# Kernel tuning notes

Measured on AMD Instinct MI355X. Metric: run time of the kernel, lower is better.

## Reference

```python
import jax, jax.numpy as jnp
import numpy as np

EPS = 1e-8  # matches F.cosine_similarity default eps


def setup_inputs() -> dict:
    key = jax.random.key(0)
    k1, k2, k3 = jax.random.split(key, 3)
    B, C, H, W = 16, 256, 64, 64
    n_e = 1024
    z = jax.random.normal(k1, (B, C, H, W), dtype=jnp.float32)
    gt = jax.random.normal(k2, (B, C, H, W), dtype=jnp.float32)
    codebook = jax.random.normal(k3, (n_e, C), dtype=jnp.float32)
    return {"z": z, "gt": gt, "codebook": codebook}


def _sq_dist(x, cb):
    return (jnp.sum(x * x, axis=1, keepdims=True)
            + jnp.sum(cb * cb, axis=1)
            - 2.0 * x @ cb.T)


def reference(z, gt, codebook):
    B, C, H, W = z.shape
    # permute to (B,H,W,C) then flatten to (N, e_dim)
    zf = jnp.transpose(z, (0, 2, 3, 1)).reshape(-1, C)
    gf = jnp.transpose(gt, (0, 2, 3, 1)).reshape(-1, C)

    idx = jnp.argmin(_sq_dist(zf, codebook), axis=1)       # [N]
    idx_gt = jnp.argmin(_sq_dist(gf, codebook), axis=1)    # [N]

    # one-hot @ codebook == direct gather
    z_q = codebook[idx].reshape(B, H, W, C)
    z_q_gt = codebook[idx_gt].reshape(B, H, W, C)

    # F.cosine_similarity(z_q_gt, z_q, dim=1) on (B,H,W,C): reduces over H -> (B,W,C)
    num = jnp.sum(z_q_gt * z_q, axis=1)
    nx = jnp.maximum(jnp.sqrt(jnp.sum(z_q_gt * z_q_gt, axis=1)), EPS)
    ny = jnp.maximum(jnp.sqrt(jnp.sum(z_q * z_q, axis=1)), EPS)
    cosine_score = num / (nx * ny)                         # (B, W, C)

    return cosine_score, idx_gt[:, None], idx[:, None]
```

## Files before the change

### kernel.cpp

```cpp
#include <hip/hip_runtime.h>

typedef _Float16 f16x8 __attribute__((ext_vector_type(8)));
typedef float f32x4 __attribute__((ext_vector_type(4)));

#define CDIM 256
#define NE 1024
#define HW 4096
#define CHW 1048576
#define OUT_COS 262144
#define N_PIX 65536
#define NT 32
#define TAU 0.1f

#define XROW_DW 260
#define XS_DW   (16 * XROW_DW)


__global__ void prep_kernel(const float* __restrict__ cb,
                            _Float16* __restrict__ hi,
                            float* __restrict__ c2f,
                            double* __restrict__ c2d) {
    int code = blockIdx.x;
    int lane = threadIdx.x;
    int t = code >> 5, sub = (code >> 4) & 1, n = code & 15;
    const float* row = cb + code * CDIM;
    double s = 0.0;
    #pragma unroll
    for (int i = 0; i < 4; ++i) {
        int d = i * 64 + lane;
        float x = row[d];
        s += (double)x * (double)x;
        int f = d >> 5, q = (d >> 3) & 3, r = d & 7;
        hi[(size_t)t * 8192 + sub * 4096 + f * 512 + q * 128 + n * 8 + r] =
            (_Float16)x;
    }
    #pragma unroll
    for (int off = 32; off > 0; off >>= 1)
        s += __shfl_down(s, off, 64);
    if (lane == 0) { c2f[code] = (float)(0.5 * s); c2d[code] = 0.5 * s; }
}

__device__ __forceinline__ void gl_lds16(const void* g, void* l) {
    __builtin_amdgcn_global_load_lds(
        (const __attribute__((address_space(1))) unsigned int*)g,
        (__attribute__((address_space(3))) unsigned int*)l, 16, 0, 0);
}

__launch_bounds__(256, 2)
__global__ void argmin_kernel(const float* __restrict__ Z,
                              const float* __restrict__ GT,
                              const _Float16* __restrict__ ghi,
                              const float* __restrict__ cb,
                              const float* __restrict__ c2f,
                              const double* __restrict__ c2d,
                              float* __restrict__ out_z,
                              float* __restrict__ out_gt) {
    __shared__ __align__(16) char smem[2 * 16640 + 4096 + 1024];
    float*    xs   = (float*)smem;
    _Float16* lbuf = (_Float16*)smem;
    float*    c2s  = (float*)(smem + 33280);
    int*      cand = (int*)(smem + 37376);

    const int wave = threadIdx.x >> 6;
    const int lane = threadIdx.x & 63;
    const int l15 = lane & 15;
    const int quad = lane >> 4;
    const int half = blockIdx.x >> 8;
    const float* X = half ? GT : Z;
    float* out_idx = half ? out_gt : out_z;
    const int p0 = (blockIdx.x & 255) * 256;

    #pragma unroll
    for (int i = 0; i < 4; ++i)
        c2s[i * 256 + threadIdx.x] = c2f[i * 256 + threadIdx.x];

    const float* xsrc = X + (size_t)(p0 >> 12) * CHW + (p0 & 4095);

    auto stage_x = [&](int b, int fr) {
        #pragma unroll
        for (int i = 0; i < 4; ++i) {
            const int rr = wave * 4 + i;
            const int d = fr * 16 + rr;
            gl_lds16(xsrc + (size_t)d * HW + lane * 4,
                     xs + b * XS_DW + rr * XROW_DW);
        }
    };

    f16x8 nah[4][8];
    stage_x(0, 0);
    int xb = 0;
    #pragma unroll
    for (int fr = 0; fr < 16; ++fr) {
        __syncthreads();
        if (fr < 15) stage_x(xb ^ 1, fr + 1);
        if ((quad >> 1) == (fr & 1)) {
            const int f = fr >> 1;
            const float* xsb = xs + xb * XS_DW;
            const int abase = (quad & 1) * 8 * XROW_DW + wave * 64 + l15;
            #pragma unroll
            for (int g = 0; g < 4; ++g) {
                f16x8 tv;
                #pragma unroll
                for (int j = 0; j < 8; ++j)
                    tv[j] = -(_Float16)xsb[abase + j * XROW_DW + g * 16];
                nah[g][f] = tv;
            }
        }
        xb ^= 1;
    }
    __syncthreads();

    int b1[4][4], b2[4][4];
    #pragma unroll
    for (int g = 0; g < 4; ++g)
        #pragma unroll
        for (int r = 0; r < 4; ++r) { b1[g][r] = 0x7fffffff; b2[g][r] = 0x7fffffff; }

    auto stage = [&](int b, int t) {
        #pragma unroll
        for (int i = 0; i < 4; ++i) {
            const int c = wave * 4 + i;
            gl_lds16(ghi + (size_t)t * 8192 + c * 512 + lane * 8,
                     lbuf + b * 8192 + c * 512);
        }
    };

    stage(0, 0);
    __syncthreads();

    for (int t = 0; t < NT; ++t) {
        const int cur = t & 1;
        if (t < NT - 1) stage(cur ^ 1, t + 1);

        #pragma unroll
        for (int sub = 0; sub < 2; ++sub) {
            const int n = t * 32 + sub * 16 + l15;
            const float c2 = c2s[n];
            f32x4 acc[4];
            #pragma unroll
            for (int g = 0; g < 4; ++g)
                acc[g] = (f32x4){c2, c2, c2, c2};

            #pragma unroll
            for (int f = 0; f < 8; ++f) {
                f16x8 bh = *(const f16x8*)&lbuf[cur * 8192 + sub * 4096 + f * 512 + lane * 8];
                acc[0] = __builtin_amdgcn_mfma_f32_16x16x32_f16(nah[0][f], bh, acc[0], 0, 0, 0);
                acc[1] = __builtin_amdgcn_mfma_f32_16x16x32_f16(nah[1][f], bh, acc[1], 0, 0, 0);
                acc[2] = __builtin_amdgcn_mfma_f32_16x16x32_f16(nah[2][f], bh, acc[2], 0, 0, 0);
                acc[3] = __builtin_amdgcn_mfma_f32_16x16x32_f16(nah[3][f], bh, acc[3], 0, 0, 0);
            }

            #pragma unroll
            for (int g = 0; g < 4; ++g) {
                #pragma unroll
                for (int r = 0; r < 4; ++r) {
                    int k = (__float_as_int(acc[g][r]) & 0xFFFFFC00) | n;
                    int mx = max(b1[g][r], k);
                    b2[g][r] = min(b2[g][r], mx);
                    b1[g][r] = min(b1[g][r], k);
                }
            }
        }
        __syncthreads();
    }

    #pragma unroll
    for (int g = 0; g < 4; ++g) {
        #pragma unroll
        for (int r = 0; r < 4; ++r) {
            int x1 = b1[g][r], x2 = b2[g][r];
            #pragma unroll
            for (int off = 8; off > 0; off >>= 1) {
                int o1 = __shfl_xor(x1, off, 64);
                int o2 = __shfl_xor(x2, off, 64);
                int tt = max(x1, o1);
                x2 = min(min(x2, o2), tt);
                x1 = min(x1, o1);
            }
            if (l15 == 0) {
                const int i1 = x1 & 1023, i2 = x2 & 1023;
                const float s1 = __int_as_float(x1 & 0xFFFFFC00);
                const float s2 = __int_as_float(x2 & 0xFFFFFC00);
                const int row = quad * 4 + r;
                const int slot = g * 16 + row;
                const bool flag = (s2 - s1) < TAU;
                cand[wave * 64 + slot] = i1 | (i2 << 10) | (flag ? (1 << 20) : 0);
                if (!flag) out_idx[p0 + wave * 64 + slot] = (float)i1;
            }
        }
    }

    const int info = cand[wave * 64 + lane];
    if (info & (1 << 20)) {
        const int i1 = info & 1023, i2 = (info >> 10) & 1023;
        const int p = p0 + wave * 64 + lane;
        const float* xb2 = X + (size_t)(p >> 12) * CHW + (p & 4095);
        const float* r1 = cb + (size_t)i1 * CDIM;
        const float* r2 = cb + (size_t)i2 * CDIM;
        double d1 = 0.0, d2 = 0.0;
        #pragma unroll 4
        for (int d = 0; d < CDIM; d += 4) {
            float x0 = xb2[(size_t)(d + 0) * HW];
            float x1v = xb2[(size_t)(d + 1) * HW];
            float x2v = xb2[(size_t)(d + 2) * HW];
            float x3v = xb2[(size_t)(d + 3) * HW];
            const float4 v1 = *(const float4*)(r1 + d);
            const float4 v2 = *(const float4*)(r2 + d);
            d1 += (double)x0 * v1.x + (double)x1v * v1.y
                + (double)x2v * v1.z + (double)x3v * v1.w;
            d2 += (double)x0 * v2.x + (double)x1v * v2.y
                + (double)x2v * v2.z + (double)x3v * v2.w;
        }
        const double dd1 = c2d[i1] - d1;
        const double dd2 = c2d[i2] - d2;
        const int bi = (dd2 < dd1 || (dd2 == dd1 && i2 < i1)) ? i2 : i1;
        out_idx[p] = (float)bi;
    }
}

__global__ void cosine_kernel(const float* __restrict__ cb,
                              const float* __restrict__ idx_z_f,
                              const float* __restrict__ idx_gt_f,
                              float* __restrict__ out_cos) {
    __shared__ int s_ig[64], s_iq[64];
    const int bw = blockIdx.x;
    const int c = threadIdx.x;
    const int b = bw >> 6, w = bw & 63;
    if (c < 64) {
        s_ig[c] = (int)idx_gt_f[b * 4096 + c * 64 + w];
    } else if (c < 128) {
        int h = c - 64;
        s_iq[h] = (int)idx_z_f[b * 4096 + h * 64 + w];
    }
    __syncthreads();
    float num = 0.f, sa = 0.f, sb = 0.f;
    #pragma unroll 1
    for (int h = 0; h < 64; h += 4) {
        float av[4], bv[4];
        #pragma unroll
        for (int u = 0; u < 4; ++u) {
            av[u] = cb[s_ig[h + u] * CDIM + c];
            bv[u] = cb[s_iq[h + u] * CDIM + c];
        }
        #pragma unroll
        for (int u = 0; u < 4; ++u) {
            num += av[u] * bv[u];
            sa += av[u] * av[u];
            sb += bv[u] * bv[u];
        }
    }
    const float nx = fmaxf(sqrtf(sa), 1e-8f);
    const float ny = fmaxf(sqrtf(sb), 1e-8f);
    out_cos[bw * CDIM + c] = num / (nx * ny);
}

extern "C" void kernel_launch(void* const* d_in, const int* in_sizes, int n_in,
                              void* d_out, int out_size, void* d_ws, size_t ws_size,
                              hipStream_t stream) {
    const float* z  = (const float*)d_in[0];
    const float* gt = (const float*)d_in[1];
    const float* cb = (const float*)d_in[2];
    float* out = (float*)d_out;

    _Float16* hi = (_Float16*)d_ws;
    float*  c2f = (float*)((char*)d_ws + 512 * 1024);
    double* c2d = (double*)((char*)d_ws + 516 * 1024);

    float* out_cos    = out;
    float* out_idx_gt = out + OUT_COS;
    float* out_idx_z  = out + OUT_COS + N_PIX;

    prep_kernel<<<NE, 64, 0, stream>>>(cb, hi, c2f, c2d);
    argmin_kernel<<<512, 256, 0, stream>>>(z, gt, hi, cb, c2f, c2d,
                                           out_idx_z, out_idx_gt);
    cosine_kernel<<<1024, 256, 0, stream>>>(cb, out_idx_z, out_idx_gt, out_cos);
}
```

Baseline: 229.0 us.

## Split codebook scan across two wave groups per block and merge top-2

```diff
diff --git a/kernel.cpp b/kernel.cpp
--- a/kernel.cpp
+++ b/kernel.cpp
@@ -9,7 +9,7 @@
 #define CHW 1048576
 #define OUT_COS 262144
 #define N_PIX 65536
-#define NT 32
+#define NTH 16
 #define TAU 0.1f
 
 #define XROW_DW 260
@@ -46,7 +46,7 @@
         (__attribute__((address_space(3))) unsigned int*)l, 16, 0, 0);
 }
 
-__launch_bounds__(256, 2)
+__launch_bounds__(512, 2)
 __global__ void argmin_kernel(const float* __restrict__ Z,
                               const float* __restrict__ GT,
                               const _Float16* __restrict__ ghi,
@@ -55,34 +55,38 @@
                               const double* __restrict__ c2d,
                               float* __restrict__ out_z,
                               float* __restrict__ out_gt) {
-    __shared__ __align__(16) char smem[2 * 16640 + 4096 + 1024];
-    float*    xs   = (float*)smem;
-    _Float16* lbuf = (_Float16*)smem;
-    float*    c2s  = (float*)(smem + 33280);
-    int*      cand = (int*)(smem + 37376);
-
-    const int wave = threadIdx.x >> 6;
-    const int lane = threadIdx.x & 63;
-    const int l15 = lane & 15;
+    __shared__ __align__(16) char smem[65536 + 4096 + 2048 + 2048];
+    float*    xs    = (float*)smem;
+    _Float16* lbuf  = (_Float16*)smem;
+    float*    c2s   = (float*)(smem + 65536);
+    int*      cand1 = (int*)(smem + 69632);
+    int*      cand2 = (int*)(smem + 71680);
+
+    const int tid  = threadIdx.x;
+    const int wave = tid >> 6;
+    const int lane = tid & 63;
+    const int l15  = lane & 15;
     const int quad = lane >> 4;
-    const int half = blockIdx.x >> 8;
-    const float* X = half ? GT : Z;
-    float* out_idx = half ? out_gt : out_z;
+    const int pw   = wave & 3;
+    const int ch   = wave >> 2;
+    const int inp  = blockIdx.x >> 8;
+    const float* X = inp ? GT : Z;
+    float* out_idx = inp ? out_gt : out_z;
     const int p0 = (blockIdx.x & 255) * 256;
 
     #pragma unroll
-    for (int i = 0; i < 4; ++i)
-        c2s[i * 256 + threadIdx.x] = c2f[i * 256 + threadIdx.x];
+    for (int i = 0; i < 2; ++i)
+        c2s[i * 512 + tid] = c2f[i * 512 + tid];
 
     const float* xsrc = X + (size_t)(p0 >> 12) * CHW + (p0 & 4095);
 
     auto stage_x = [&](int b, int fr) {
         #pragma unroll
-        for (int i = 0; i < 4; ++i) {
-            const int rr = wave * 4 + i;
+        for (int i = 0; i < 2; ++i) {
+            const int rr = wave * 2 + i;
             const int d = fr * 16 + rr;
             gl_lds16(xsrc + (size_t)d * HW + lane * 4,
-                     xs + b * XS_DW + rr * XROW_DW);
+                     xs + b * (XS_DW / 1) + rr * XROW_DW);
         }
     };
 
@@ -96,7 +100,7 @@
         if ((quad >> 1) == (fr & 1)) {
             const int f = fr >> 1;
             const float* xsb = xs + xb * XS_DW;
-            const int abase = (quad & 1) * 8 * XROW_DW + wave * 64 + l15;
+            const int abase = (quad & 1) * 8 * XROW_DW + pw * 64 + l15;
             #pragma unroll
             for (int g = 0; g < 4; ++g) {
                 f16x8 tv;
@@ -119,22 +123,22 @@
     auto stage = [&](int b, int t) {
         #pragma unroll
         for (int i = 0; i < 4; ++i) {
-            const int c = wave * 4 + i;
-            gl_lds16(ghi + (size_t)t * 8192 + c * 512 + lane * 8,
-                     lbuf + b * 8192 + c * 512);
+            const int c = pw * 4 + i;
+            gl_lds16(ghi + (size_t)(ch * NTH + t) * 8192 + c * 512 + lane * 8,
+                     lbuf + (ch * 2 + b) * 8192 + c * 512);
         }
     };
 
     stage(0, 0);
     __syncthreads();
 
-    for (int t = 0; t < NT; ++t) {
+    for (int t = 0; t < NTH; ++t) {
         const int cur = t & 1;
-        if (t < NT - 1) stage(cur ^ 1, t + 1);
+        if (t < NTH - 1) stage(cur ^ 1, t + 1);
 
         #pragma unroll
         for (int sub = 0; sub < 2; ++sub) {
-            const int n = t * 32 + sub * 16 + l15;
+            const int n = ch * 512 + t * 32 + sub * 16 + l15;
             const float c2 = c2s[n];
             f32x4 acc[4];
             #pragma unroll
@@ -143,7 +147,8 @@
 
             #pragma unroll
             for (int f = 0; f < 8; ++f) {
-                f16x8 bh = *(const f16x8*)&lbuf[cur * 8192 + sub * 4096 + f * 512 + lane * 8];
+                f16x8 bh = *(const f16x8*)
+                    &lbuf[(ch * 2 + cur) * 8192 + sub * 4096 + f * 512 + lane * 8];
                 acc[0] = __builtin_amdgcn_mfma_f32_16x16x32_f16(nah[0][f], bh, acc[0], 0, 0, 0);
                 acc[1] = __builtin_amdgcn_mfma_f32_16x16x32_f16(nah[1][f], bh, acc[1], 0, 0, 0);
                 acc[2] = __builtin_amdgcn_mfma_f32_16x16x32_f16(nah[2][f], bh, acc[2], 0, 0, 0);
@@ -178,43 +183,50 @@
                 x1 = min(x1, o1);
             }
             if (l15 == 0) {
-                const int i1 = x1 & 1023, i2 = x2 & 1023;
-                const float s1 = __int_as_float(x1 & 0xFFFFFC00);
-                const float s2 = __int_as_float(x2 & 0xFFFFFC00);
                 const int row = quad * 4 + r;
-                const int slot = g * 16 + row;
-                const bool flag = (s2 - s1) < TAU;
-                cand[wave * 64 + slot] = i1 | (i2 << 10) | (flag ? (1 << 20) : 0);
-                if (!flag) out_idx[p0 + wave * 64 + slot] = (float)i1;
-            }
-        }
-    }
-
-    const int info = cand[wave * 64 + lane];
-    if (info & (1 << 20)) {
-        const int i1 = info & 1023, i2 = (info >> 10) & 1023;
-        const int p = p0 + wave * 64 + lane;
-        const float* xb2 = X + (size_t)(p >> 12) * CHW + (p & 4095);
-        const float* r1 = cb + (size_t)i1 * CDIM;
-        const float* r2 = cb + (size_t)i2 * CDIM;
-        double d1 = 0.0, d2 = 0.0;
-        #pragma unroll 4
-        for (int d = 0; d < CDIM; d += 4) {
-            float x0 = xb2[(size_t)(d + 0) * HW];
-            float x1v = xb2[(size_t)(d + 1) * HW];
-            float x2v = xb2[(size_t)(d + 2) * HW];
-            float x3v = xb2[(size_t)(d + 3) * HW];
-            const float4 v1 = *(const float4*)(r1 + d);
-            const float4 v2 = *(const float4*)(r2 + d);
-            d1 += (double)x0 * v1.x + (double)x1v * v1.y
-                + (double)x2v * v1.z + (double)x3v * v1.w;
-            d2 += (double)x0 * v2.x + (double)x1v * v2.y
-                + (double)x2v * v2.z + (double)x3v * v2.w;
-        }
-        const double dd1 = c2d[i1] - d1;
-        const double dd2 = c2d[i2] - d2;
-        const int bi = (dd2 < dd1 || (dd2 == dd1 && i2 < i1)) ? i2 : i1;
-        out_idx[p] = (float)bi;
+                const int px = pw * 64 + g * 16 + row;
+                cand1[ch * 256 + px] = x1;
+                cand2[ch * 256 + px] = x2;
+            }
+        }
+    }
+    __syncthreads();
+
+    if (tid < 256) {
+        const int px = tid;
+        const int a1 = cand1[px],       a2 = cand2[px];
+        const int c1 = cand1[256 + px], c2k = cand2[256 + px];
+        const int m1 = min(a1, c1);
+        const int m2 = min(min(a2, c2k), max(a1, c1));
+        const int i1 = m1 & 1023, i2 = m2 & 1023;
+        const float s1 = __int_as_float(m1 & 0xFFFFFC00);
+        const float s2 = __int_as_float(m2 & 0xFFFFFC00);
+        const int p = p0 + px;
+        if ((s2 - s1) >= TAU) {
+            out_idx[p] = (float)i1;
+        } else {
+            const float* xb2 = X + (size_t)(p >> 12) * CHW + (p & 4095);
+            const float* r1 = cb + (size_t)i1 * CDIM;
+            const float* r2 = cb + (size_t)i2 * CDIM;
+            double d1 = 0.0, d2 = 0.0;
+            #pragma unroll 4
+            for (int d = 0; d < CDIM; d += 4) {
+                float x0 = xb2[(size_t)(d + 0) * HW];
+                float x1v = xb2[(size_t)(d + 1) * HW];
+                float x2v = xb2[(size_t)(d + 2) * HW];
+                float x3v = xb2[(size_t)(d + 3) * HW];
+                const float4 v1 = *(const float4*)(r1 + d);
+                const float4 v2 = *(const float4*)(r2 + d);
+                d1 += (double)x0 * v1.x + (double)x1v * v1.y
+                    + (double)x2v * v1.z + (double)x3v * v1.w;
+                d2 += (double)x0 * v2.x + (double)x1v * v2.y
+                    + (double)x2v * v2.z + (double)x3v * v2.w;
+            }
+            const double dd1 = c2d[i1] - d1;
+            const double dd2 = c2d[i2] - d2;
+            const int bi = (dd2 < dd1 || (dd2 == dd1 && i2 < i1)) ? i2 : i1;
+            out_idx[p] = (float)bi;
+        }
     }
 }
 
@@ -271,7 +283,7 @@
     float* out_idx_z  = out + OUT_COS + N_PIX;
 
     prep_kernel<<<NE, 64, 0, stream>>>(cb, hi, c2f, c2d);
-    argmin_kernel<<<512, 256, 0, stream>>>(z, gt, hi, cb, c2f, c2d,
+    argmin_kernel<<<512, 512, 0, stream>>>(z, gt, hi, cb, c2f, c2d,
                                            out_idx_z, out_idx_gt);
     cosine_kernel<<<1024, 256, 0, stream>>>(cb, out_idx_z, out_idx_gt, out_cos);
 }
```

Result: slower. 239.7 us (+4.7%).

## Triple-buffer LDS staging with vmcnt waits and a single barrier per step

Applied to the files above, without the earlier changes.

```diff
diff --git a/kernel.cpp b/kernel.cpp
--- a/kernel.cpp
+++ b/kernel.cpp
@@ -13,7 +13,7 @@
 #define TAU 0.1f
 
 #define XROW_DW 260
-#define XS_DW   (16 * XROW_DW)
+#define XS_DW   4160
 
 
 __global__ void prep_kernel(const float* __restrict__ cb,
@@ -55,11 +55,11 @@
                               const double* __restrict__ c2d,
                               float* __restrict__ out_z,
                               float* __restrict__ out_gt) {
-    __shared__ __align__(16) char smem[2 * 16640 + 4096 + 1024];
+    __shared__ __align__(16) char smem[55040];
     float*    xs   = (float*)smem;
     _Float16* lbuf = (_Float16*)smem;
-    float*    c2s  = (float*)(smem + 33280);
-    int*      cand = (int*)(smem + 37376);
+    float*    c2s  = (float*)(smem + 49920);
+    int*      cand = (int*)(smem + 54016);
 
     const int wave = threadIdx.x >> 6;
     const int lane = threadIdx.x & 63;
@@ -88,14 +88,19 @@
 
     f16x8 nah[4][8];
     stage_x(0, 0);
-    int xb = 0;
     #pragma unroll
     for (int fr = 0; fr < 16; ++fr) {
-        __syncthreads();
-        if (fr < 15) stage_x(xb ^ 1, fr + 1);
+        if (fr < 15) {
+            stage_x((fr + 1) % 3, fr + 1);
+            asm volatile("s_waitcnt vmcnt(4)" ::: "memory");
+        } else {
+            asm volatile("s_waitcnt vmcnt(0)" ::: "memory");
+        }
+        __builtin_amdgcn_s_barrier();
+        __builtin_amdgcn_sched_barrier(0);
         if ((quad >> 1) == (fr & 1)) {
             const int f = fr >> 1;
-            const float* xsb = xs + xb * XS_DW;
+            const float* xsb = xs + (fr % 3) * XS_DW;
             const int abase = (quad & 1) * 8 * XROW_DW + wave * 64 + l15;
             #pragma unroll
             for (int g = 0; g < 4; ++g) {
@@ -106,7 +111,6 @@
                 nah[g][f] = tv;
             }
         }
-        xb ^= 1;
     }
     __syncthreads();
 
@@ -126,11 +130,17 @@
     };
 
     stage(0, 0);
-    __syncthreads();
-
+    int cur = 0;
     for (int t = 0; t < NT; ++t) {
-        const int cur = t & 1;
-        if (t < NT - 1) stage(cur ^ 1, t + 1);
+        const int nxt = (cur == 2) ? 0 : cur + 1;
+        if (t < NT - 1) {
+            stage(nxt, t + 1);
+            asm volatile("s_waitcnt vmcnt(4)" ::: "memory");
+        } else {
+            asm volatile("s_waitcnt vmcnt(0)" ::: "memory");
+        }
+        __builtin_amdgcn_s_barrier();
+        __builtin_amdgcn_sched_barrier(0);
 
         #pragma unroll
         for (int sub = 0; sub < 2; ++sub) {
@@ -143,7 +153,8 @@
 
             #pragma unroll
             for (int f = 0; f < 8; ++f) {
-                f16x8 bh = *(const f16x8*)&lbuf[cur * 8192 + sub * 4096 + f * 512 + lane * 8];
+                f16x8 bh = *(const f16x8*)
+                    &lbuf[cur * 8192 + sub * 4096 + f * 512 + lane * 8];
                 acc[0] = __builtin_amdgcn_mfma_f32_16x16x32_f16(nah[0][f], bh, acc[0], 0, 0, 0);
                 acc[1] = __builtin_amdgcn_mfma_f32_16x16x32_f16(nah[1][f], bh, acc[1], 0, 0, 0);
                 acc[2] = __builtin_amdgcn_mfma_f32_16x16x32_f16(nah[2][f], bh, acc[2], 0, 0, 0);
@@ -161,7 +172,7 @@
                 }
             }
         }
-        __syncthreads();
+        cur = nxt;
     }
 
     #pragma unroll
```

Result: slower. 233.7 us (+2.1%).
